# Kernel optimization log

Hardware: AMD Instinct MI355X
Metric: run time of the kernel (lower is better)

## Reference

```python
import jax, jax.numpy as jnp
import numpy as np

B, LQ, LS, S = 64, 64, 512, 512
NEG = -1e6


def mask_for_lengths(lengths, max_len, mask_right=True):
    pos = jnp.arange(max_len)
    if mask_right:
        m = pos[None, :] >= lengths[:, None]
    else:
        m = pos[None, :] < lengths[:, None]
    return jnp.where(m, jnp.float32(NEG), jnp.float32(0.0))


def setup_inputs() -> dict:
    key = jax.random.key(0)
    ks = jax.random.split(key, 12)
    f = lambda k, shp: jax.random.normal(k, shp, jnp.float32)
    sc = np.float32(1.0 / np.sqrt(S))
    return {
        "encoded_question": f(ks[0], (B, LQ, S)),
        "encoded_support": f(ks[1], (B, LS, S)),
        "question_length": jax.random.randint(ks[2], (B,), 1, LQ + 1),
        "support_length": jax.random.randint(ks[3], (B,), LS // 2, LS + 1),
        "correct_start": jax.random.randint(ks[4], (B,), 0, LS),
        "answer2question": jnp.arange(B),
        "is_eval": 1,
        "W_qa": f(ks[5], (S, 1)) * sc,
        "W_qsi": f(ks[6], (S, S)) * sc,
        "b_qsi": jnp.zeros((S,), jnp.float32),
        "W_qs": f(ks[7], (2 * S, S)) * sc,
        "W_ss": f(ks[8], (S, 1)) * sc,
        "W_qei": f(ks[9], (S, S)) * sc,
        "b_qei": jnp.zeros((S,), jnp.float32),
        "W_qe": f(ks[10], (3 * S, S)) * sc,
        "W_es": f(ks[11], (S, 1)) * sc,
    }


def reference(encoded_question, encoded_support, question_length, support_length,
              correct_start, answer2question, is_eval,
              W_qa, W_qsi, b_qsi, W_qs, W_ss, W_qei, b_qei, W_qe, W_es):
    # question attention pooling
    att = jnp.einsum('bqd,do->bq', encoded_question, W_qa)
    att = att + mask_for_lengths(question_length, LQ)
    w = jax.nn.softmax(att, axis=1)                                   # [B,LQ]
    q_state = jnp.einsum('bqd,bq->bd', encoded_question, w)           # [B,S]

    # start scoring
    start_input = jnp.concatenate(
        [q_state[:, None, :] * encoded_support, encoded_support], axis=2)  # [B,LS,2S]
    q_start_inter = q_state @ W_qsi + b_qsi                           # [B,S]
    q_start_state = start_input @ W_qs + q_start_inter[:, None, :]    # [B,LS,S]
    support_mask = mask_for_lengths(support_length, LS)
    start_scores = jnp.einsum('bld,do->bl', jax.nn.relu(q_start_state), W_ss)
    start_scores = start_scores + support_mask                        # [B,LS]
    predicted_start_pointer = jnp.argmax(start_scores, axis=1)        # [B]

    # eval path: start_pointer = predicted argmax
    start_pointer = predicted_start_pointer
    u_s = jnp.take_along_axis(encoded_support,
                              start_pointer[:, None, None], axis=1)[:, 0, :]  # [B,S]

    # end scoring
    end_input = jnp.concatenate(
        [encoded_support * u_s[:, None, :], start_input], axis=2)     # [B,LS,3S]
    q_end_inter = q_state @ W_qei + b_qei
    q_end_state = end_input @ W_qe + q_end_inter[:, None, :]          # [B,LS,S]
    end_scores = jnp.einsum('bld,do->bl', jax.nn.relu(q_end_state), W_es)
    end_scores = end_scores + support_mask
    # eval: mask positions left of start_pointer
    end_scores = end_scores + mask_for_lengths(start_pointer, LS, mask_right=False)
    predicted_end_pointer = jnp.argmax(end_scores, axis=1)

    return (start_scores, end_scores, predicted_start_pointer, predicted_end_pointer)
```

## Files before the change

### kernel.cpp

```cpp
#include <hip/hip_runtime.h>
#include <math.h>

constexpr int B_  = 64;
constexpr int LQ_ = 64;
constexpr int LS_ = 512;
constexpr int S_  = 512;
#define NEGV (-1e6f)
#define MARGIN 0.0625f

typedef __attribute__((ext_vector_type(8))) short bf16x8;
typedef __attribute__((ext_vector_type(4))) float f32x4;

__device__ inline unsigned short f2bf_rn(float x) {
    unsigned u = __builtin_bit_cast(unsigned, x);
    unsigned r = (u + 0x7FFFu + ((u >> 16) & 1u)) >> 16;
    return (unsigned short)r;
}

__global__ __launch_bounds__(512)
void qpool_inter_kernel(const float* __restrict__ eq, const int* __restrict__ qlen,
                        const float* __restrict__ W_qa,
                        const float* __restrict__ W_qsi, const float* __restrict__ b_qsi,
                        const float* __restrict__ W_qei, const float* __restrict__ b_qei,
                        float* __restrict__ q_state,
                        float* __restrict__ qsi, float* __restrict__ qei)
{
    int b = blockIdx.x;
    int which = blockIdx.y;
    const float* W  = which ? W_qei : W_qsi;
    const float* bi = which ? b_qei : b_qsi;
    float*       o  = which ? qei   : qsi;

    int t = threadIdx.x, lane = t & 63, w = t >> 6;
    __shared__ float att[LQ_], wsm[LQ_], qs[S_];
    __shared__ float red[8][S_];
    const float* eqb = eq + (size_t)b * LQ_ * S_;

    #pragma unroll
    for (int k = 0; k < 8; ++k) {
        int q = w + 8 * k;
        const float* row = eqb + q * S_;
        float s = 0.f;
        #pragma unroll
        for (int j = 0; j < 8; ++j)
            s = fmaf(row[lane + 64 * j], W_qa[lane + 64 * j], s);
        #pragma unroll
        for (int off = 32; off >= 1; off >>= 1)
            s += __shfl_xor(s, off);
        if (lane == 0) att[q] = s;
    }
    __syncthreads();

    if (w == 0) {
        int L = qlen[b];
        float v = att[lane] + ((lane < L) ? 0.f : NEGV);
        float m = v;
        #pragma unroll
        for (int off = 32; off >= 1; off >>= 1)
            m = fmaxf(m, __shfl_xor(m, off));
        float e = expf(v - m);
        float sum = e;
        #pragma unroll
        for (int off = 32; off >= 1; off >>= 1)
            sum += __shfl_xor(sum, off);
        wsm[lane] = e / sum;
    }
    __syncthreads();

    {
        float acc = 0.f;
        #pragma unroll 8
        for (int q = 0; q < LQ_; ++q)
            acc = fmaf(wsm[q], eqb[q * S_ + t], acc);
        qs[t] = acc;
        if (which == 0) q_state[b * S_ + t] = acc;
    }
    __syncthreads();

    {
        float z[8];
        #pragma unroll
        for (int k = 0; k < 8; ++k) z[k] = 0.f;
        const int d0 = w * 64;
        #pragma unroll 4
        for (int dd = 0; dd < 64; ++dd) {
            int d = d0 + dd;
            float q = qs[d];
            const float* row = W + (size_t)d * S_ + lane;
            #pragma unroll
            for (int k = 0; k < 8; ++k)
                z[k] = fmaf(q, row[k * 64], z[k]);
        }
        #pragma unroll
        for (int k = 0; k < 8; ++k) red[w][k * 64 + lane] = z[k];
    }
    __syncthreads();
    {
        float acc = bi[t];
        #pragma unroll
        for (int ww = 0; ww < 8; ++ww) acc += red[ww][t];
        o[b * S_ + t] = acc;
    }
}

template <int NT>
__global__ __launch_bounds__(512)
void prep_kernel(const float* __restrict__ W, const float* __restrict__ q_state,
                 const float* __restrict__ u_s, short* __restrict__ Wc)
{
    int bid = blockIdx.x;
    int i = bid >> 6, b = bid & 63;
    int col = threadIdx.x;
    __shared__ float scq[32], scu[32];
    if (col < 32) scq[col] = q_state[b * S_ + i * 32 + col];
    if (NT == 3 && col >= 32 && col < 64) scu[col - 32] = u_s[b * S_ + i * 32 + col - 32];
    __syncthreads();

    unsigned short h[32];
    #pragma unroll
    for (int d = 0; d < 32; ++d) {
        int D = i * 32 + d;
        float v;
        if (NT == 2)
            v = fmaf(scq[d], W[(size_t)D * S_ + col], W[(size_t)(S_ + D) * S_ + col]);
        else
            v = fmaf(scu[d], W[(size_t)D * S_ + col],
                fmaf(scq[d], W[(size_t)(S_ + D) * S_ + col], W[(size_t)(2 * S_ + D) * S_ + col]));
        h[d] = f2bf_rn(v);
    }
    size_t base = (size_t)b * 262144 + (size_t)i * 16384 + (size_t)col * 8;
    #pragma unroll
    for (int kc = 0; kc < 4; ++kc) {
        uint4 H;
        H.x = h[kc*8+0] | ((unsigned)h[kc*8+1] << 16);
        H.y = h[kc*8+2] | ((unsigned)h[kc*8+3] << 16);
        H.z = h[kc*8+4] | ((unsigned)h[kc*8+5] << 16);
        H.w = h[kc*8+6] | ((unsigned)h[kc*8+7] << 16);
        *(uint4*)&Wc[base + kc * 4096] = H;
    }
}

template <bool END>
__global__ __launch_bounds__(512)
void score_kernel(const float* __restrict__ es, const short* __restrict__ Wc,
                  const float* __restrict__ inter, const float* __restrict__ Wsmall,
                  const int* __restrict__ slen, const int* __restrict__ sp,
                  float* __restrict__ out)
{
    const int t = threadIdx.x;
    const int lane = t & 63, wid = t >> 6;
    const int wr = wid >> 2, wc = wid & 3;
    const int l15 = lane & 15, l4 = lane >> 4;

    int lid = blockIdx.x;
    int xcd = lid & 7, slot = lid >> 3;
    int b  = xcd * 8 + (slot >> 2);
    int rc = slot & 3;

    __shared__ __attribute__((aligned(16))) short As[2][4096];
    __shared__ __attribute__((aligned(16))) short Bs[2][16384];
    __shared__ float int_l[S_], wsm_l[S_];
    __shared__ float sm_red[128][4];

    int_l[t] = inter[b * S_ + t];
    wsm_l[t] = Wsmall[t];

    const char* Bbase = (const char*)(Wc + (size_t)b * 262144);

    f32x4 acc[4][8];
    #pragma unroll
    for (int r = 0; r < 4; ++r)
        #pragma unroll
        for (int c = 0; c < 8; ++c)
            acc[r][c] = (f32x4){0.f, 0.f, 0.f, 0.f};

    const int arow = t >> 2, akc = t & 3;
    const float* aptr = es + ((size_t)(b * LS_ + rc * 128 + arow)) * S_ + akc * 8;

    auto stageB = [&](int i, int buf) {
        const char* gb = Bbase + (size_t)i * 32768 + t * 16;
        char* lb = (char*)Bs[buf] + t * 16;
        #pragma unroll
        for (int q = 0; q < 4; ++q)
            __builtin_amdgcn_global_load_lds(
                (const __attribute__((address_space(1))) void*)(gb + q * 8192),
                (__attribute__((address_space(3))) void*)(lb + q * 8192), 16, 0, 0);
    };
    auto buildA = [&](int buf, float4 a0, float4 a1) {
        uint4 HA;
        HA.x = f2bf_rn(a0.x) | ((unsigned)f2bf_rn(a0.y) << 16);
        HA.y = f2bf_rn(a0.z) | ((unsigned)f2bf_rn(a0.w) << 16);
        HA.z = f2bf_rn(a1.x) | ((unsigned)f2bf_rn(a1.y) << 16);
        HA.w = f2bf_rn(a1.z) | ((unsigned)f2bf_rn(a1.w) << 16);
        *(uint4*)&As[buf][akc * 1024 + arow * 8] = HA;
    };

    float4 s0 = *(const float4*)(aptr);
    float4 s1 = *(const float4*)(aptr + 4);
    buildA(0, s0, s1);
    stageB(0, 0);
    float4 n0 = *(const float4*)(aptr + 32);
    float4 n1 = *(const float4*)(aptr + 36);

    for (int i = 0; i < 16; ++i) {
        const int buf = i & 1;
        if (i + 1 < 16) {
            stageB(i + 1, buf ^ 1);
            buildA(buf ^ 1, n0, n1);
            if (i + 2 < 16) {
                n0 = *(const float4*)(aptr + (i + 2) * 32);
                n1 = *(const float4*)(aptr + (i + 2) * 32 + 4);
            }
            asm volatile("s_waitcnt vmcnt(4) lgkmcnt(0)" ::: "memory");
        } else {
            asm volatile("s_waitcnt vmcnt(0) lgkmcnt(0)" ::: "memory");
        }
        __builtin_amdgcn_s_barrier();

        bf16x8 ah[4];
        #pragma unroll
        for (int r = 0; r < 4; ++r) {
            int rowp = wr * 64 + r * 16 + l15;
            ah[r] = *(const bf16x8*)&As[buf][l4 * 1024 + rowp * 8];
        }
        #pragma unroll
        for (int c = 0; c < 8; ++c) {
            int col = wc * 128 + c * 16 + l15;
            bf16x8 bh = *(const bf16x8*)&Bs[buf][l4 * 4096 + col * 8];
            #pragma unroll
            for (int r = 0; r < 4; ++r)
                acc[r][c] = __builtin_amdgcn_mfma_f32_16x16x32_bf16(ah[r], bh, acc[r][c], 0, 0, 0);
        }
        asm volatile("s_waitcnt lgkmcnt(0)" ::: "memory");
        __builtin_amdgcn_s_barrier();
    }

    #pragma unroll
    for (int r = 0; r < 4; ++r) {
        #pragma unroll
        for (int jj = 0; jj < 4; ++jj) {
            float pr = 0.f;
            #pragma unroll
            for (int c = 0; c < 8; ++c) {
                int col = wc * 128 + c * 16 + l15;
                float v = acc[r][c][jj] + int_l[col];
                v = fmaxf(v, 0.f);
                pr = fmaf(v, wsm_l[col], pr);
            }
            pr += __shfl_xor(pr, 1);
            pr += __shfl_xor(pr, 2);
            pr += __shfl_xor(pr, 4);
            pr += __shfl_xor(pr, 8);
            if (l15 == 0) sm_red[wr * 64 + r * 16 + l4 * 4 + jj][wc] = pr;
        }
    }
    __syncthreads();
    if (t < 128) {
        int l = rc * 128 + t;
        float s = sm_red[t][0] + sm_red[t][1] + sm_red[t][2] + sm_red[t][3];
        if (l >= slen[b]) s += NEGV;
        if (END) { if (l < sp[b]) s += NEGV; }
        out[b * LS_ + l] = s;
    }
}

__device__ inline int select_cands(const float* s_l, int t, int lane, int w,
                                   float* wred, int* wcnt, int* cand)
{
    float v = s_l[t];
    #pragma unroll
    for (int off = 32; off >= 1; off >>= 1)
        v = fmaxf(v, __shfl_xor(v, off));
    if (lane == 0) wred[w] = v;
    __syncthreads();
    float m = wred[0];
    #pragma unroll
    for (int k = 1; k < 8; ++k) m = fmaxf(m, wred[k]);
    float th = m - MARGIN;
    bool flag = s_l[t] >= th;
    unsigned long long bal = __ballot(flag);
    int rank = __popcll(bal & ((1ull << lane) - 1ull));
    if (lane == 0) wcnt[w] = (int)__popcll(bal);
    __syncthreads();
    int off = 0, total = 0;
    #pragma unroll
    for (int k = 0; k < 8; ++k) { if (k < w) off += wcnt[k]; total += wcnt[k]; }
    if (flag) { int pos = off + rank; if (pos < 8) cand[pos] = t; }
    __syncthreads();
    return total < 8 ? total : 8;
}

template <bool END>
__global__ __launch_bounds__(512)
void rescue_kernel(const float* __restrict__ support, const float* __restrict__ q_state,
                   const float* __restrict__ u_s_in, const float* __restrict__ Wbig,
                   const float* __restrict__ inter, const float* __restrict__ Wsmall,
                   const float* __restrict__ scores, float* __restrict__ part)
{
    int bid = blockIdx.x;
    int b = bid >> 3, cslot = bid & 7;
    int t = threadIdx.x, lane = t & 63, w = t >> 6;
    __shared__ float s_l[S_], qs_l[S_], us_l[S_], arow_sh[S_];
    __shared__ float red[8][S_];
    __shared__ float wred[8];
    __shared__ int wcnt[8], cand[8];

    s_l[t]  = scores[b * S_ + t];
    qs_l[t] = q_state[b * S_ + t];
    if (END) us_l[t] = u_s_in[b * S_ + t];
    __syncthreads();

    int cnt = select_cands(s_l, t, lane, w, wred, wcnt, cand);
    if (cnt == 1 || cslot >= cnt) return;

    int ci = cand[cslot];
    arow_sh[t] = support[((size_t)(b * LS_ + ci)) * S_ + t];
    __syncthreads();

    const float* W1 = Wbig;
    const float* W2 = Wbig + (size_t)S_ * S_;
    const float* W3 = Wbig + (size_t)2 * S_ * S_;
    const int d0 = w * 64;

    float z[8];
    #pragma unroll
    for (int j = 0; j < 8; ++j) z[j] = 0.f;

    #pragma unroll 2
    for (int dd = 0; dd < 64; ++dd) {
        int d = d0 + dd;
        float a  = arow_sh[d];
        float qa = qs_l[d] * a;
        float ua = END ? us_l[d] * a : 0.f;
        const float* r1 = W1 + (size_t)d * S_ + lane;
        const float* r2 = W2 + (size_t)d * S_ + lane;
        const float* r3 = W3 + (size_t)d * S_ + lane;
        #pragma unroll
        for (int j = 0; j < 8; ++j) {
            if (END)
                z[j] = fmaf(ua, r1[64 * j], fmaf(qa, r2[64 * j], fmaf(a, r3[64 * j], z[j])));
            else
                z[j] = fmaf(qa, r1[64 * j], fmaf(a, r2[64 * j], z[j]));
        }
    }
    #pragma unroll
    for (int j = 0; j < 8; ++j) red[w][lane + 64 * j] = z[j];
    __syncthreads();

    float v = 0.f;
    #pragma unroll
    for (int ww = 0; ww < 8; ++ww) v += red[ww][t];
    float p = fmaxf(v + inter[b * S_ + t], 0.f) * Wsmall[t];
    #pragma unroll
    for (int off = 32; off >= 1; off >>= 1)
        p += __shfl_xor(p, off);
    if (lane == 0) wred[w] = p;
    __syncthreads();
    if (t == 0) {
        float e = ((wred[0] + wred[1]) + (wred[2] + wred[3])) +
                  ((wred[4] + wred[5]) + (wred[6] + wred[7]));
        part[b * 8 + cslot] = e;
    }
}

template <bool END>
__global__ __launch_bounds__(512)
void finalize_kernel(const float* __restrict__ scores, const float* __restrict__ part,
                     const float* __restrict__ support, int* __restrict__ sp_ws,
                     float* __restrict__ pred, float* __restrict__ us_out)
{
    int b = blockIdx.x;
    int t = threadIdx.x, lane = t & 63, w = t >> 6;
    __shared__ float s_l[S_];
    __shared__ float wred[8];
    __shared__ int wcnt[8], cand[8];
    __shared__ int best_sh;

    s_l[t] = scores[b * S_ + t];
    __syncthreads();
    int cnt = select_cands(s_l, t, lane, w, wred, wcnt, cand);

    if (t == 0) {
        int bi = cand[0];
        if (cnt > 1) {
            float bv = -INFINITY;
            for (int c = 0; c < cnt; ++c) {
                float e = part[b * 8 + c];
                if (e > bv) { bv = e; bi = cand[c]; }
            }
        }
        best_sh = bi;
        pred[b] = (float)bi;
        if (!END) sp_ws[b] = bi;
    }
    __syncthreads();
    if (!END)
        us_out[b * S_ + t] = support[((size_t)(b * LS_ + best_sh)) * S_ + t];
}

extern "C" void kernel_launch(void* const* d_in, const int* in_sizes, int n_in,
                              void* d_out, int out_size, void* d_ws, size_t ws_size,
                              hipStream_t stream)
{
    const float* eq    = (const float*)d_in[0];
    const float* es    = (const float*)d_in[1];
    const int*   qlen  = (const int*)d_in[2];
    const int*   slen  = (const int*)d_in[3];
    const float* W_qa  = (const float*)d_in[7];
    const float* W_qsi = (const float*)d_in[8];
    const float* b_qsi = (const float*)d_in[9];
    const float* W_qs  = (const float*)d_in[10];
    const float* W_ss  = (const float*)d_in[11];
    const float* W_qei = (const float*)d_in[12];
    const float* b_qei = (const float*)d_in[13];
    const float* W_qe  = (const float*)d_in[14];
    const float* W_es  = (const float*)d_in[15];

    float* out          = (float*)d_out;
    float* start_scores = out;
    float* end_scores   = out + B_ * LS_;
    float* pred_start   = out + 2 * B_ * LS_;
    float* pred_end     = out + 2 * B_ * LS_ + B_;

    float* ws      = (float*)d_ws;
    float* q_state = ws;
    float* qsi     = ws + B_ * S_;
    float* qei     = ws + 2 * B_ * S_;
    float* u_s     = ws + 3 * B_ * S_;
    float* part    = ws + 4 * B_ * S_;
    int*   sp_ws   = (int*)(ws + 4 * B_ * S_ + 512);
    short* Wc      = (short*)(ws + 4 * B_ * S_ + 1024);

    qpool_inter_kernel<<<dim3(B_, 2), 512, 0, stream>>>(
        eq, qlen, W_qa, W_qsi, b_qsi, W_qei, b_qei, q_state, qsi, qei);

    prep_kernel<2><<<1024, 512, 0, stream>>>(W_qs, q_state, nullptr, Wc);
    score_kernel<false><<<256, 512, 0, stream>>>(es, Wc, qsi, W_ss, slen, nullptr, start_scores);
    rescue_kernel<false><<<B_ * 8, 512, 0, stream>>>(es, q_state, nullptr, W_qs, qsi, W_ss,
                                                     start_scores, part);
    finalize_kernel<false><<<B_, 512, 0, stream>>>(start_scores, part, es, sp_ws, pred_start, u_s);

    prep_kernel<3><<<1024, 512, 0, stream>>>(W_qe, q_state, u_s, Wc);
    score_kernel<true><<<256, 512, 0, stream>>>(es, Wc, qei, W_es, slen, sp_ws, end_scores);
    rescue_kernel<true><<<B_ * 8, 512, 0, stream>>>(es, q_state, u_s, W_qe, qei, W_es,
                                                    end_scores, part);
    finalize_kernel<true><<<B_, 512, 0, stream>>>(end_scores, part, es, nullptr, pred_end, nullptr);
}
```

Baseline: 169.3 us.

## Fuse start finalize into end prep and register-stage B tiles in score kernel

The start-pointer finalize step is merged into the end-weight prep kernel. Every prep block redoes the candidate selection and gathers the u_s row straight from the support tensor, which removes one launch and the u_s workspace buffer. The end rescue kernel now reads u_s from support through the stored start pointer. Separately, the score kernel stops using async global_load_lds for the B tiles and instead loads them into registers two stages ahead, then writes them to LDS in an unrolled pair of buffers. This trades higher register pressure and redundant selection work across 16 blocks per batch for fewer launches and a different load pipeline.

Result: faster. 162.9 us (-3.8%).

```diff
diff --git a/kernel.cpp b/kernel.cpp
--- a/kernel.cpp
+++ b/kernel.cpp
@@ -103,29 +103,48 @@
     }
 }
 
-template <int NT>
+__device__ inline int select_cands(const float* s_l, int t, int lane, int w,
+                                   float* wred, int* wcnt, int* cand)
+{
+    float v = s_l[t];
+    #pragma unroll
+    for (int off = 32; off >= 1; off >>= 1)
+        v = fmaxf(v, __shfl_xor(v, off));
+    if (lane == 0) wred[w] = v;
+    __syncthreads();
+    float m = wred[0];
+    #pragma unroll
+    for (int k = 1; k < 8; ++k) m = fmaxf(m, wred[k]);
+    float th = m - MARGIN;
+    bool flag = s_l[t] >= th;
+    unsigned long long bal = __ballot(flag);
+    int rank = __popcll(bal & ((1ull << lane) - 1ull));
+    if (lane == 0) wcnt[w] = (int)__popcll(bal);
+    __syncthreads();
+    int off = 0, total = 0;
+    #pragma unroll
+    for (int k = 0; k < 8; ++k) { if (k < w) off += wcnt[k]; total += wcnt[k]; }
+    if (flag) { int pos = off + rank; if (pos < 8) cand[pos] = t; }
+    __syncthreads();
+    return total < 8 ? total : 8;
+}
+
 __global__ __launch_bounds__(512)
-void prep_kernel(const float* __restrict__ W, const float* __restrict__ q_state,
-                 const float* __restrict__ u_s, short* __restrict__ Wc)
+void prep_start_kernel(const float* __restrict__ W, const float* __restrict__ q_state,
+                       short* __restrict__ Wc)
 {
     int bid = blockIdx.x;
     int i = bid >> 6, b = bid & 63;
     int col = threadIdx.x;
-    __shared__ float scq[32], scu[32];
+    __shared__ float scq[32];
     if (col < 32) scq[col] = q_state[b * S_ + i * 32 + col];
-    if (NT == 3 && col >= 32 && col < 64) scu[col - 32] = u_s[b * S_ + i * 32 + col - 32];
     __syncthreads();
 
     unsigned short h[32];
     #pragma unroll
     for (int d = 0; d < 32; ++d) {
         int D = i * 32 + d;
-        float v;
-        if (NT == 2)
-            v = fmaf(scq[d], W[(size_t)D * S_ + col], W[(size_t)(S_ + D) * S_ + col]);
-        else
-            v = fmaf(scu[d], W[(size_t)D * S_ + col],
-                fmaf(scq[d], W[(size_t)(S_ + D) * S_ + col], W[(size_t)(2 * S_ + D) * S_ + col]));
+        float v = fmaf(scq[d], W[(size_t)D * S_ + col], W[(size_t)(S_ + D) * S_ + col]);
         h[d] = f2bf_rn(v);
     }
     size_t base = (size_t)b * 262144 + (size_t)i * 16384 + (size_t)col * 8;
@@ -140,6 +159,68 @@
     }
 }
 
+__global__ __launch_bounds__(512)
+void prep_end_kernel(const float* __restrict__ W, const float* __restrict__ q_state,
+                     const float* __restrict__ es, const float* __restrict__ start_scores,
+                     const float* __restrict__ part,
+                     int* __restrict__ sp_ws, float* __restrict__ pred_start,
+                     short* __restrict__ Wc)
+{
+    int bid = blockIdx.x;
+    int i = bid >> 6, b = bid & 63;
+    int t = threadIdx.x, lane = t & 63, w = t >> 6;
+    __shared__ float s_l[S_];
+    __shared__ float wred[8];
+    __shared__ int wcnt[8], cand[8];
+    __shared__ float scq[32], scu[32];
+    __shared__ int best_sh;
+
+    s_l[t] = start_scores[b * S_ + t];
+    __syncthreads();
+    int cnt = select_cands(s_l, t, lane, w, wred, wcnt, cand);
+
+    if (t == 0) {
+        int bi = cand[0];
+        if (cnt > 1) {
+            float bv = -INFINITY;
+            for (int c = 0; c < cnt; ++c) {
+                float e = part[b * 8 + c];
+                if (e > bv) { bv = e; bi = cand[c]; }
+            }
+        }
+        best_sh = bi;
+        if (i == 0) { pred_start[b] = (float)bi; sp_ws[b] = bi; }
+    }
+    __syncthreads();
+    int best = best_sh;
+
+    if (t < 32) scq[t] = q_state[b * S_ + i * 32 + t];
+    if (t >= 32 && t < 64)
+        scu[t - 32] = es[((size_t)(b * LS_ + best)) * S_ + i * 32 + (t - 32)];
+    __syncthreads();
+
+    int col = t;
+    unsigned short h[32];
+    #pragma unroll
+    for (int d = 0; d < 32; ++d) {
+        int D = i * 32 + d;
+        float v = fmaf(scu[d], W[(size_t)D * S_ + col],
+                  fmaf(scq[d], W[(size_t)(S_ + D) * S_ + col],
+                       W[(size_t)(2 * S_ + D) * S_ + col]));
+        h[d] = f2bf_rn(v);
+    }
+    size_t base = (size_t)b * 262144 + (size_t)i * 16384 + (size_t)col * 8;
+    #pragma unroll
+    for (int kc = 0; kc < 4; ++kc) {
+        uint4 H;
+        H.x = h[kc*8+0] | ((unsigned)h[kc*8+1] << 16);
+        H.y = h[kc*8+2] | ((unsigned)h[kc*8+3] << 16);
+        H.z = h[kc*8+4] | ((unsigned)h[kc*8+5] << 16);
+        H.w = h[kc*8+6] | ((unsigned)h[kc*8+7] << 16);
+        *(uint4*)&Wc[base + kc * 4096] = H;
+    }
+}
+
 template <bool END>
 __global__ __launch_bounds__(512)
 void score_kernel(const float* __restrict__ es, const short* __restrict__ Wc,
@@ -177,15 +258,6 @@
     const int arow = t >> 2, akc = t & 3;
     const float* aptr = es + ((size_t)(b * LS_ + rc * 128 + arow)) * S_ + akc * 8;
 
-    auto stageB = [&](int i, int buf) {
-        const char* gb = Bbase + (size_t)i * 32768 + t * 16;
-        char* lb = (char*)Bs[buf] + t * 16;
-        #pragma unroll
-        for (int q = 0; q < 4; ++q)
-            __builtin_amdgcn_global_load_lds(
-                (const __attribute__((address_space(1))) void*)(gb + q * 8192),
-                (__attribute__((address_space(3))) void*)(lb + q * 8192), 16, 0, 0);
-    };
     auto buildA = [&](int buf, float4 a0, float4 a1) {
         uint4 HA;
         HA.x = f2bf_rn(a0.x) | ((unsigned)f2bf_rn(a0.y) << 16);
@@ -194,29 +266,7 @@
         HA.w = f2bf_rn(a1.z) | ((unsigned)f2bf_rn(a1.w) << 16);
         *(uint4*)&As[buf][akc * 1024 + arow * 8] = HA;
     };
-
-    float4 s0 = *(const float4*)(aptr);
-    float4 s1 = *(const float4*)(aptr + 4);
-    buildA(0, s0, s1);
-    stageB(0, 0);
-    float4 n0 = *(const float4*)(aptr + 32);
-    float4 n1 = *(const float4*)(aptr + 36);
-
-    for (int i = 0; i < 16; ++i) {
-        const int buf = i & 1;
-        if (i + 1 < 16) {
-            stageB(i + 1, buf ^ 1);
-            buildA(buf ^ 1, n0, n1);
-            if (i + 2 < 16) {
-                n0 = *(const float4*)(aptr + (i + 2) * 32);
-                n1 = *(const float4*)(aptr + (i + 2) * 32 + 4);
-            }
-            asm volatile("s_waitcnt vmcnt(4) lgkmcnt(0)" ::: "memory");
-        } else {
-            asm volatile("s_waitcnt vmcnt(0) lgkmcnt(0)" ::: "memory");
-        }
-        __builtin_amdgcn_s_barrier();
-
+    auto mfma_step = [&](int buf) {
         bf16x8 ah[4];
         #pragma unroll
         for (int r = 0; r < 4; ++r) {
@@ -231,8 +281,71 @@
             for (int r = 0; r < 4; ++r)
                 acc[r][c] = __builtin_amdgcn_mfma_f32_16x16x32_bf16(ah[r], bh, acc[r][c], 0, 0, 0);
         }
+    };
+
+    uint4 P0, P1, P2, P3, Q0, Q1, Q2, Q3;
+    {
+        const char* gb = Bbase + t * 16;
+        P0 = *(const uint4*)(gb);
+        P1 = *(const uint4*)(gb + 8192);
+        P2 = *(const uint4*)(gb + 16384);
+        P3 = *(const uint4*)(gb + 24576);
+        const char* gb1 = gb + 32768;
+        Q0 = *(const uint4*)(gb1);
+        Q1 = *(const uint4*)(gb1 + 8192);
+        Q2 = *(const uint4*)(gb1 + 16384);
+        Q3 = *(const uint4*)(gb1 + 24576);
+    }
+    float4 pa0 = *(const float4*)(aptr);
+    float4 pa1 = *(const float4*)(aptr + 4);
+    float4 qa0 = *(const float4*)(aptr + 32);
+    float4 qa1 = *(const float4*)(aptr + 36);
+
+    #pragma unroll 1
+    for (int ii = 0; ii < 8; ++ii) {
+        const int i = ii * 2;
+
+        {
+            char* lb = (char*)Bs[0] + t * 16;
+            *(uint4*)(lb)         = P0;
+            *(uint4*)(lb + 8192)  = P1;
+            *(uint4*)(lb + 16384) = P2;
+            *(uint4*)(lb + 24576) = P3;
+        }
+        buildA(0, pa0, pa1);
+        if (i + 2 < 16) {
+            const char* gb = Bbase + (size_t)(i + 2) * 32768 + t * 16;
+            P0 = *(const uint4*)(gb);
+            P1 = *(const uint4*)(gb + 8192);
+            P2 = *(const uint4*)(gb + 16384);
+            P3 = *(const uint4*)(gb + 24576);
+            pa0 = *(const float4*)(aptr + (i + 2) * 32);
+            pa1 = *(const float4*)(aptr + (i + 2) * 32 + 4);
+        }
         asm volatile("s_waitcnt lgkmcnt(0)" ::: "memory");
         __builtin_amdgcn_s_barrier();
+        mfma_step(0);
+
+        {
+            char* lb = (char*)Bs[1] + t * 16;
+            *(uint4*)(lb)         = Q0;
+            *(uint4*)(lb + 8192)  = Q1;
+            *(uint4*)(lb + 16384) = Q2;
+            *(uint4*)(lb + 24576) = Q3;
+        }
+        buildA(1, qa0, qa1);
+        if (i + 3 < 16) {
+            const char* gb = Bbase + (size_t)(i + 3) * 32768 + t * 16;
+            Q0 = *(const uint4*)(gb);
+            Q1 = *(const uint4*)(gb + 8192);
+            Q2 = *(const uint4*)(gb + 16384);
+            Q3 = *(const uint4*)(gb + 24576);
+            qa0 = *(const float4*)(aptr + (i + 3) * 32);
+            qa1 = *(const float4*)(aptr + (i + 3) * 32 + 4);
+        }
+        asm volatile("s_waitcnt lgkmcnt(0)" ::: "memory");
+        __builtin_amdgcn_s_barrier();
+        mfma_step(1);
     }
 
     #pragma unroll
@@ -264,36 +377,10 @@
     }
 }
 
-__device__ inline int select_cands(const float* s_l, int t, int lane, int w,
-                                   float* wred, int* wcnt, int* cand)
-{
-    float v = s_l[t];
-    #pragma unroll
-    for (int off = 32; off >= 1; off >>= 1)
-        v = fmaxf(v, __shfl_xor(v, off));
-    if (lane == 0) wred[w] = v;
-    __syncthreads();
-    float m = wred[0];
-    #pragma unroll
-    for (int k = 1; k < 8; ++k) m = fmaxf(m, wred[k]);
-    float th = m - MARGIN;
-    bool flag = s_l[t] >= th;
-    unsigned long long bal = __ballot(flag);
-    int rank = __popcll(bal & ((1ull << lane) - 1ull));
-    if (lane == 0) wcnt[w] = (int)__popcll(bal);
-    __syncthreads();
-    int off = 0, total = 0;
-    #pragma unroll
-    for (int k = 0; k < 8; ++k) { if (k < w) off += wcnt[k]; total += wcnt[k]; }
-    if (flag) { int pos = off + rank; if (pos < 8) cand[pos] = t; }
-    __syncthreads();
-    return total < 8 ? total : 8;
-}
-
 template <bool END>
 __global__ __launch_bounds__(512)
 void rescue_kernel(const float* __restrict__ support, const float* __restrict__ q_state,
-                   const float* __restrict__ u_s_in, const float* __restrict__ Wbig,
+                   const int* __restrict__ sp, const float* __restrict__ Wbig,
                    const float* __restrict__ inter, const float* __restrict__ Wsmall,
                    const float* __restrict__ scores, float* __restrict__ part)
 {
@@ -307,7 +394,10 @@
 
     s_l[t]  = scores[b * S_ + t];
     qs_l[t] = q_state[b * S_ + t];
-    if (END) us_l[t] = u_s_in[b * S_ + t];
+    if (END) {
+        int spv = sp[b];
+        us_l[t] = support[((size_t)(b * LS_ + spv)) * S_ + t];
+    }
     __syncthreads();
 
     int cnt = select_cands(s_l, t, lane, w, wred, wcnt, cand);
@@ -363,18 +453,15 @@
     }
 }
 
-template <bool END>
 __global__ __launch_bounds__(512)
-void finalize_kernel(const float* __restrict__ scores, const float* __restrict__ part,
-                     const float* __restrict__ support, int* __restrict__ sp_ws,
-                     float* __restrict__ pred, float* __restrict__ us_out)
+void finalize_end_kernel(const float* __restrict__ scores, const float* __restrict__ part,
+                         float* __restrict__ pred)
 {
     int b = blockIdx.x;
     int t = threadIdx.x, lane = t & 63, w = t >> 6;
     __shared__ float s_l[S_];
     __shared__ float wred[8];
     __shared__ int wcnt[8], cand[8];
-    __shared__ int best_sh;
 
     s_l[t] = scores[b * S_ + t];
     __syncthreads();
@@ -389,13 +476,8 @@
                 if (e > bv) { bv = e; bi = cand[c]; }
             }
         }
-        best_sh = bi;
         pred[b] = (float)bi;
-        if (!END) sp_ws[b] = bi;
-    }
-    __syncthreads();
-    if (!END)
-        us_out[b * S_ + t] = support[((size_t)(b * LS_ + best_sh)) * S_ + t];
+    }
 }
 
 extern "C" void kernel_launch(void* const* d_in, const int* in_sizes, int n_in,
@@ -426,23 +508,22 @@
     float* q_state = ws;
     float* qsi     = ws + B_ * S_;
     float* qei     = ws + 2 * B_ * S_;
-    float* u_s     = ws + 3 * B_ * S_;
-    float* part    = ws + 4 * B_ * S_;
-    int*   sp_ws   = (int*)(ws + 4 * B_ * S_ + 512);
-    short* Wc      = (short*)(ws + 4 * B_ * S_ + 1024);
+    float* part    = ws + 3 * B_ * S_;
+    int*   sp_ws   = (int*)(ws + 3 * B_ * S_ + 512);
+    short* Wc      = (short*)(ws + 3 * B_ * S_ + 1024);
 
     qpool_inter_kernel<<<dim3(B_, 2), 512, 0, stream>>>(
         eq, qlen, W_qa, W_qsi, b_qsi, W_qei, b_qei, q_state, qsi, qei);
 
-    prep_kernel<2><<<1024, 512, 0, stream>>>(W_qs, q_state, nullptr, Wc);
+    prep_start_kernel<<<1024, 512, 0, stream>>>(W_qs, q_state, Wc);
     score_kernel<false><<<256, 512, 0, stream>>>(es, Wc, qsi, W_ss, slen, nullptr, start_scores);
     rescue_kernel<false><<<B_ * 8, 512, 0, stream>>>(es, q_state, nullptr, W_qs, qsi, W_ss,
                                                      start_scores, part);
-    finalize_kernel<false><<<B_, 512, 0, stream>>>(start_scores, part, es, sp_ws, pred_start, u_s);
-
-    prep_kernel<3><<<1024, 512, 0, stream>>>(W_qe, q_state, u_s, Wc);
+
+    prep_end_kernel<<<1024, 512, 0, stream>>>(W_qe, q_state, es, start_scores, part,
+                                              sp_ws, pred_start, Wc);
     score_kernel<true><<<256, 512, 0, stream>>>(es, Wc, qei, W_es, slen, sp_ws, end_scores);
-    rescue_kernel<true><<<B_ * 8, 512, 0, stream>>>(es, q_state, u_s, W_qe, qei, W_es,
+    rescue_kernel<true><<<B_ * 8, 512, 0, stream>>>(es, q_state, sp_ws, W_qe, qei, W_es,
                                                     end_scores, part);
-    finalize_kernel<true><<<B_, 512, 0, stream>>>(end_scores, part, es, nullptr, pred_end, nullptr);
-}
+    finalize_end_kernel<<<B_, 512, 0, stream>>>(end_scores, part, pred_end);
+}
```
